# Kernel optimization log

Measured on AMD Instinct MI355X. Metric: run time of the kernel, lower is better.

Reference implementation:

```python
import jax, jax.numpy as jnp
import numpy as np

CIN, COUT, R, N, B = 4, 4, 4, 4096, 32

def setup_inputs() -> dict:
    key = jax.random.key(0)
    k1, k2, k3 = jax.random.split(key, 3)
    x = jax.random.normal(k1, (CIN, B, N), dtype=jnp.float32)
    # torch.nn.init.normal(std=0.01)
    G = 0.01 * jax.random.normal(k2, (CIN, COUT, R, N), dtype=jnp.float32)
    H = 0.01 * jax.random.normal(k3, (CIN, COUT, R, N), dtype=jnp.float32)
    return {"x": x, "G": G, "H": H}

def reference(x, G, H):
    """LDR layer, displacement='toep_corner' (cycle=True).

    For each channel pair (i,j):
        M_ij = sum_s C_1(G[i,j,s]) @ C_{-1}(H[i,j,s])^T
    where C_f(v) is the f-circulant matrix with first column v
    (= Krylov matrix of the f-unit-circulant shift Z_f with vector v).
    out[j] = sum_i M_ij @ x[i]^T  (batched over batch dim).

    Identities used (F = DFT):
      C_1(u) y      = ifft(fft(u) * fft(y))
      C_1(u)^T y    = fft(fft(u) * ifft(y))
      C_f(v)        = D^{-1} C_1(D v) D,  D = diag(zeta^k), zeta = f^{1/n}
      => C_{-1}(h)^T y = D * fft(fft(D*h) * ifft(conj(D)*y)), D_k = exp(i*pi*k/n)
    All channel pairs and ranks are batched in a single FFT call (no Python
    loops over channels, unlike the original double loop).
    """
    cin, b, n = x.shape
    k = jnp.arange(n)
    D = jnp.exp(1j * jnp.pi * k / n).astype(jnp.complex64)   # zeta^k for f=-1
    Dinv = jnp.conj(D)

    # --- step 1: t[i,j,s,b,:] = C_{-1}(H[i,j,s])^T x[i,b,:]  -> (cin,cout,r,b,n)
    Hf = jnp.fft.fft(D * H.astype(jnp.complex64), axis=-1)           # (cin,cout,r,n)
    Xf = jnp.fft.ifft(Dinv * x.astype(jnp.complex64), axis=-1)       # (cin,b,n)
    t = D * jnp.fft.fft(Hf[:, :, :, None, :] * Xf[:, None, None, :, :], axis=-1)

    # --- step 2: out[j,b,:] = Re ifft( sum_{i,s} fft(G[i,j,s]) * fft(t[i,j,s,b]) )
    Gf = jnp.fft.fft(G, axis=-1).astype(jnp.complex64)               # (cin,cout,r,n)
    Tf = jnp.fft.fft(t, axis=-1)                                     # (cin,cout,r,b,n)
    Yf = jnp.einsum('ijsn,ijsbn->jbn', Gf, Tf)                       # (cout,b,n)
    return jnp.real(jnp.fft.ifft(Yf, axis=-1)).astype(x.dtype)
```

## Files before the change

### kernel.cpp

```cpp
#include <hip/hip_runtime.h>
#include <hip/hip_fp16.h>
#include <math.h>


#define NFFT  4096
#define NT    256
#define CIN   4
#define COUT  4
#define RANK  4
#define BATCH 32
#define PI_F  3.14159265358979323846f

constexpr float CP16[16] = {
    1.0000000000000000f,  0.9807852804032304f,  0.9238795325112867f,  0.8314696123025452f,
    0.7071067811865476f,  0.5555702330196022f,  0.3826834323650898f,  0.1950903220161282f,
    0.0000000000000000f, -0.1950903220161282f, -0.3826834323650898f, -0.5555702330196022f,
   -0.7071067811865476f, -0.8314696123025452f, -0.9238795325112867f, -0.9807852804032304f };
constexpr float SP16[16] = {
    0.0000000000000000f,  0.1950903220161282f,  0.3826834323650898f,  0.5555702330196022f,
    0.7071067811865476f,  0.8314696123025452f,  0.9238795325112867f,  0.9807852804032304f,
    1.0000000000000000f,  0.9807852804032304f,  0.9238795325112867f,  0.8314696123025452f,
    0.7071067811865476f,  0.5555702330196022f,  0.3826834323650898f,  0.1950903220161282f };

__device__ __forceinline__ float2 cmul(float2 a, float2 b) {
    return make_float2(a.x*b.x - a.y*b.y, a.x*b.y + a.y*b.x);
}
__device__ __forceinline__ float2 cadd(float2 a, float2 b){ return make_float2(a.x+b.x, a.y+b.y); }
__device__ __forceinline__ float2 csub(float2 a, float2 b){ return make_float2(a.x-b.x, a.y-b.y); }

__device__ __forceinline__ int SW(int e){ return e ^ ((e >> 4) & 15); }

template<int SIGN>
__device__ __forceinline__ void dft16(float2 v[16]) {
    const float sgn = (float)SIGN;
    const float C8 = 0.923879532511287f, S8 = 0.382683432365090f, H2 = 0.707106781186548f;
    const float2 w1 = make_float2( C8,  sgn*S8);
    const float2 w2 = make_float2( H2,  sgn*H2);
    const float2 w3 = make_float2( S8,  sgn*C8);
    const float2 w4 = make_float2(0.f,  sgn);
    const float2 w6 = make_float2(-H2,  sgn*H2);
    const float2 w9 = make_float2(-C8, -sgn*S8);
    float2 t[16];
    #pragma unroll
    for (int p = 0; p < 4; ++p) {
        float2 a0 = v[p], a1 = v[p+4], a2 = v[p+8], a3 = v[p+12];
        float2 b0 = cadd(a0,a2), b1 = csub(a0,a2), b2 = cadd(a1,a3), b3 = csub(a1,a3);
        float2 ib3 = make_float2(-sgn*b3.y, sgn*b3.x);
        float2 X0 = cadd(b0,b2), X2c = csub(b0,b2);
        float2 X1 = cadd(b1,ib3), X3 = csub(b1,ib3);
        if (p == 1) { X1 = cmul(X1,w1); X2c = cmul(X2c,w2); X3 = cmul(X3,w3); }
        else if (p == 2) { X1 = cmul(X1,w2); X2c = cmul(X2c,w4); X3 = cmul(X3,w6); }
        else if (p == 3) { X1 = cmul(X1,w3); X2c = cmul(X2c,w6); X3 = cmul(X3,w9); }
        t[4*p+0]=X0; t[4*p+1]=X1; t[4*p+2]=X2c; t[4*p+3]=X3;
    }
    #pragma unroll
    for (int q = 0; q < 4; ++q) {
        float2 a0 = t[q], a1 = t[q+4], a2 = t[q+8], a3 = t[q+12];
        float2 b0 = cadd(a0,a2), b1 = csub(a0,a2), b2 = cadd(a1,a3), b3 = csub(a1,a3);
        float2 ib3 = make_float2(-sgn*b3.y, sgn*b3.x);
        v[q+0]  = cadd(b0,b2);
        v[q+8]  = csub(b0,b2);
        v[q+4]  = cadd(b1,ib3);
        v[q+12] = csub(b1,ib3);
    }
}

__device__ __forceinline__ void twiddle16(float2 v[16], float ang) {
    float sn, cs; __sincosf(ang, &sn, &cs);
    float2 w  = make_float2(cs, sn);
    float2 w2 = cmul(w, w);
    float2 to = w;
    float2 te = w2;
    v[1] = cmul(v[1], to);
    v[2] = cmul(v[2], te);
    #pragma unroll
    for (int k = 3; k < 16; k += 2) {
        to = cmul(to, w2); v[k] = cmul(v[k], to);
        if (k + 1 < 16) { te = cmul(te, w2); v[k+1] = cmul(v[k+1], te); }
    }
}

__device__ __forceinline__ void twiddle16_pair(float2 v0[16], float2 v1[16], float ang) {
    float sn, cs; __sincosf(ang, &sn, &cs);
    float2 w  = make_float2(cs, sn);
    float2 w2 = cmul(w, w);
    float2 to = w;
    float2 te = w2;
    v0[1] = cmul(v0[1], to); v1[1] = cmul(v1[1], to);
    v0[2] = cmul(v0[2], te); v1[2] = cmul(v1[2], te);
    #pragma unroll
    for (int k = 3; k < 16; k += 2) {
        to = cmul(to, w2); v0[k] = cmul(v0[k], to); v1[k] = cmul(v1[k], to);
        if (k + 1 < 16) { te = cmul(te, w2); v0[k+1] = cmul(v0[k+1], te); v1[k+1] = cmul(v1[k+1], te); }
    }
}

template<int SIGN>
__device__ void fft4096_r16(float2 v[16], float2* lds, int tid) {
    dft16<SIGN>(v);
    twiddle16(v, (float)SIGN * 2.0f * PI_F * (float)tid / 4096.0f);
    #pragma unroll
    for (int k = 0; k < 16; ++k) lds[SW(16*tid + k)] = v[k];
    __syncthreads();
    #pragma unroll
    for (int r = 0; r < 16; ++r) v[r] = lds[SW(tid + 256*r)];
    dft16<SIGN>(v);
    twiddle16(v, (float)SIGN * 2.0f * PI_F * (float)(tid >> 4) / 256.0f);
    __syncthreads();
    {
        const int q = tid & 15, p = tid >> 4;
        #pragma unroll
        for (int k = 0; k < 16; ++k) lds[SW(q + 256*p + 16*k)] = v[k];
    }
    __syncthreads();
    #pragma unroll
    for (int r = 0; r < 16; ++r) v[r] = lds[SW(tid + 256*r)];
    dft16<SIGN>(v);
    __syncthreads();
}

template<int SIGN>
__device__ void fft4096_pair(float2 v0[16], float2 v1[16],
                             float2* lds0, float2* lds1, int tid) {
    dft16<SIGN>(v0);
    dft16<SIGN>(v1);
    twiddle16_pair(v0, v1, (float)SIGN * 2.0f * PI_F * (float)tid / 4096.0f);
    #pragma unroll
    for (int k = 0; k < 16; ++k) {
        const int a = SW(16*tid + k);
        lds0[a] = v0[k]; lds1[a] = v1[k];
    }
    __syncthreads();
    #pragma unroll
    for (int r = 0; r < 16; ++r) {
        const int a = SW(tid + 256*r);
        v0[r] = lds0[a]; v1[r] = lds1[a];
    }
    dft16<SIGN>(v0);
    dft16<SIGN>(v1);
    twiddle16_pair(v0, v1, (float)SIGN * 2.0f * PI_F * (float)(tid >> 4) / 256.0f);
    __syncthreads();
    {
        const int q = tid & 15, p = tid >> 4;
        #pragma unroll
        for (int k = 0; k < 16; ++k) {
            const int a = SW(q + 256*p + 16*k);
            lds0[a] = v0[k]; lds1[a] = v1[k];
        }
    }
    __syncthreads();
    #pragma unroll
    for (int r = 0; r < 16; ++r) {
        const int a = SW(tid + 256*r);
        v0[r] = lds0[a]; v1[r] = lds1[a];
    }
    dft16<SIGN>(v0);
    dft16<SIGN>(v1);
    __syncthreads();
}

__global__ __launch_bounds__(NT, 2) void ldr_pre_k(
    const float* __restrict__ x, const float* __restrict__ G, const float* __restrict__ H,
    float2* __restrict__ Hc, float2* __restrict__ Gf, float2* __restrict__ Xf)
{
    __shared__ float2 lds[NFFT];
    const int tid = threadIdx.x;
    const int bid = blockIdx.x;
    float2 v[16];
    if (bid < 32) {
        const float* h0 = H + (size_t)(2*bid)     * NFFT;
        const float* h1 = H + (size_t)(2*bid + 1) * NFFT;
        float sn, cs; __sincosf(PI_F * (float)tid / (float)NFFT, &sn, &cs);
        const float2 dt = make_float2(cs, sn);
        #pragma unroll
        for (int k = 0; k < 16; ++k) {
            const int e = tid + 256*k;
            const float2 d = cmul(dt, make_float2(CP16[k], SP16[k]));
            v[k] = cmul(d, make_float2(h0[e], h1[e]));
        }
        fft4096_r16<-1>(v, lds, tid);
        float2* o = Hc + (size_t)bid * NFFT;
        #pragma unroll
        for (int k = 0; k < 16; ++k) o[tid + 256*k] = v[k];
    } else if (bid < 96) {
        const int row = bid - 32;
        const float* g = G + (size_t)row * NFFT;
        #pragma unroll
        for (int k = 0; k < 16; ++k) v[k] = make_float2(g[tid + 256*k], 0.0f);
        fft4096_r16<-1>(v, lds, tid);
        float2* o = Gf + (size_t)row * NFFT;
        #pragma unroll
        for (int k = 0; k < 16; ++k) o[tid + 256*k] = v[k];
    } else {
        const int row = bid - 96;
        const float* xp = x + (size_t)row * NFFT;
        float sn, cs; __sincosf(PI_F * (float)tid / (float)NFFT, &sn, &cs);
        const float2 dt = make_float2(cs, -sn);
        #pragma unroll
        for (int k = 0; k < 16; ++k) {
            const int e = tid + 256*k;
            const float2 d = cmul(dt, make_float2(CP16[k], -SP16[k]));
            float xv = xp[e];
            v[k] = make_float2(d.x*xv, d.y*xv);
        }
        fft4096_r16<1>(v, lds, tid);
        const float invn = 1.0f / (float)NFFT;
        float2* o = Xf + (size_t)row * NFFT;
        #pragma unroll
        for (int k = 0; k < 16; ++k) o[tid + 256*k] = make_float2(v[k].x*invn, v[k].y*invn);
    }
}

__global__ __launch_bounds__(NT, 2) void ldr_mid_k(
    const float2* __restrict__ Hc, const float2* __restrict__ Xf,
    const float2* __restrict__ Gf, __half2* __restrict__ Ph)
{
    __shared__ float2 lds0[NFFT];
    __shared__ float2 lds1[NFFT];
    const int tid = threadIdx.x;
    const int bid = blockIdx.x;
    const int bp  = bid & 15;
    const int ip  = bid >> 4;
    const int pr  = ip & 1;
    const int ij  = ip >> 1;
    const int i   = ij >> 2;
    const int j   = ij & 3;
    const int r0  = ij*RANK + 2*pr;
    const int b0  = 2*bp;
    const float2* hc = Hc + (size_t)ip * NFFT;
    const float2* x0 = Xf + (size_t)(i*BATCH + b0) * NFFT;
    const float2* x1 = x0 + NFFT;
    const float2* g0 = Gf + (size_t)r0 * NFFT;
    const float2* g1 = g0 + NFFT;
    const int u = i*2 + pr;

    float2 v0[16], v1[16];
    #pragma unroll
    for (int k = 0; k < 16; ++k) {
        const int e = tid + 256*k;
        const float2 h = hc[e];
        v0[k] = cmul(h, x0[e]);
        v1[k] = cmul(h, x1[e]);
    }
    fft4096_pair<-1>(v0, v1, lds0, lds1, tid);
    {
        float sn, cs; __sincosf(PI_F * (float)tid / (float)NFFT, &sn, &cs);
        const float2 dt = make_float2(cs, sn);
        #pragma unroll
        for (int k = 0; k < 16; ++k) {
            const float2 d = cmul(dt, make_float2(CP16[k], SP16[k]));
            v0[k] = cmul(v0[k], d);
            v1[k] = cmul(v1[k], d);
        }
    }
    fft4096_pair<-1>(v0, v1, lds0, lds1, tid);

    #pragma unroll
    for (int k = 8; k < 16; ++k) {
        const int a = SW(tid + 256*k);
        lds0[a] = v0[k]; lds1[a] = v1[k];
    }
    __syncthreads();

    __half2* prow0 = Ph + (size_t)((u*COUT + j)*BATCH + b0) * (NFFT/2);
    __half2* prow1 = prow0 + (NFFT/2);
    #pragma unroll
    for (int k = 0; k < 8; ++k) {
        const int e = tid + 256*k;
        const float2 g0e = g0[e], g1e = g1[e];
        const int am = SW(4096 - e);
        {
            const float2 Zk = v0[k];
            const float2 Zm = (e == 0) ? Zk : lds0[am];
            const float2 V1 = make_float2(0.5f*(Zk.x + Zm.x), 0.5f*(Zk.y - Zm.y));
            const float2 V2 = make_float2(0.5f*(Zk.y + Zm.y), 0.5f*(Zm.x - Zk.x));
            float2 Y = cadd(cmul(g0e, V1), cmul(g1e, V2));
            if (k == 0 && tid == 0) {
                const float2 Zn = v0[8];
                const float Ynyq = g0[2048].x * Zn.x + g1[2048].x * Zn.y;
                Y = make_float2(Y.x, Ynyq);
            }
            prow0[e] = __floats2half2_rn(Y.x, Y.y);
        }
        {
            const float2 Zk = v1[k];
            const float2 Zm = (e == 0) ? Zk : lds1[am];
            const float2 V1 = make_float2(0.5f*(Zk.x + Zm.x), 0.5f*(Zk.y - Zm.y));
            const float2 V2 = make_float2(0.5f*(Zk.y + Zm.y), 0.5f*(Zm.x - Zk.x));
            float2 Y = cadd(cmul(g0e, V1), cmul(g1e, V2));
            if (k == 0 && tid == 0) {
                const float2 Zn = v1[8];
                const float Ynyq = g0[2048].x * Zn.x + g1[2048].x * Zn.y;
                Y = make_float2(Y.x, Ynyq);
            }
            prow1[e] = __floats2half2_rn(Y.x, Y.y);
        }
    }
}

__global__ __launch_bounds__(NT, 2) void ldr_fin_k(
    const __half2* __restrict__ Ph, float* __restrict__ out)
{
    __shared__ float2 lds[NFFT];
    __shared__ float2 sh[NFFT/2];
    const int tid = threadIdx.x;
    const int bid = blockIdx.x;
    const int b = bid & (BATCH - 1);
    const int j = bid >> 5;

    float2 a[8];
    #pragma unroll
    for (int k = 0; k < 8; ++k) a[k] = make_float2(0.f, 0.f);
    #pragma unroll
    for (int u = 0; u < 8; ++u) {
        const int4* row4 = (const int4*)(Ph + (size_t)((u*COUT + j)*BATCH + b) * (NFFT/2));
        #pragma unroll
        for (int c = 0; c < 2; ++c) {
            const int4 w = row4[tid + 256*c];
            const int ww[4] = { w.x, w.y, w.z, w.w };
            #pragma unroll
            for (int r = 0; r < 4; ++r) {
                __half2 h = *(const __half2*)&ww[r];
                float2 f = __half22float2(h);
                a[c*4+r] = cadd(a[c*4+r], f);
            }
        }
    }
    float4* sh4 = (float4*)sh;
    #pragma unroll
    for (int c = 0; c < 2; ++c) {
        sh4[2*(tid + 256*c) + 0] = make_float4(a[c*4+0].x, a[c*4+0].y, a[c*4+1].x, a[c*4+1].y);
        sh4[2*(tid + 256*c) + 1] = make_float4(a[c*4+2].x, a[c*4+2].y, a[c*4+3].x, a[c*4+3].y);
    }
    __syncthreads();

    const float dc  = sh[0].x;
    const float nyq = sh[0].y;
    float2 v[16];
    #pragma unroll
    for (int k = 0; k < 8; ++k) v[k] = sh[tid + 256*k];
    if (tid == 0) v[0] = make_float2(dc, 0.0f);
    #pragma unroll
    for (int k = 8; k < 16; ++k) {
        const int m = 4096 - (tid + 256*k);
        if (m == 2048) {
            v[k] = make_float2(nyq, 0.0f);
        } else {
            float2 c = sh[m];
            v[k] = make_float2(c.x, -c.y);
        }
    }
    fft4096_r16<1>(v, lds, tid);
    const float invn = 1.0f / (float)NFFT;
    float* orow = out + (size_t)bid * NFFT;
    #pragma unroll
    for (int k = 0; k < 16; ++k) orow[tid + 256*k] = v[k].x * invn;
}

extern "C" void kernel_launch(void* const* d_in, const int* in_sizes, int n_in,
                              void* d_out, int out_size, void* d_ws, size_t ws_size,
                              hipStream_t stream) {
    const float* x = (const float*)d_in[0];
    const float* G = (const float*)d_in[1];
    const float* H = (const float*)d_in[2];
    float* out = (float*)d_out;

    float2*  Hc = (float2*)d_ws;
    float2*  Gf = Hc + (size_t)32 * NFFT;
    float2*  Xf = Gf + (size_t)64 * NFFT;
    __half2* Ph = (__half2*)(Xf + (size_t)128 * NFFT);

    ldr_pre_k<<<224, NT, 0, stream>>>(x, G, H, Hc, Gf, Xf);
    ldr_mid_k<<<512, NT, 0, stream>>>(Hc, Xf, Gf, Ph);
    ldr_fin_k<<<COUT * BATCH, NT, 0, stream>>>(Ph, out);
}
```

Measured before the change: 93.86 us.

## Switch mid kernel to 512-thread radix-8 paired FFT

Rewrites the middle kernel's two paired 4096-point FFTs from a radix-16, 256-thread, 3-pass scheme to a radix-8, 512-thread, 4-pass scheme. Each thread now holds 8 elements per signal instead of 16, which cuts register pressure and doubles threads per block to raise occupancy and latency hiding. The cost is an extra LDS exchange pass and barrier per FFT, plus reworked indexing for the load, twiddle and real-split epilogue.

```diff
diff --git a/kernel.cpp b/kernel.cpp
--- a/kernel.cpp
+++ b/kernel.cpp
@@ -5,6 +5,7 @@
 
 #define NFFT  4096
 #define NT    256
+#define NTM   512
 #define CIN   4
 #define COUT  4
 #define RANK  4
@@ -21,6 +22,12 @@
     0.7071067811865476f,  0.8314696123025452f,  0.9238795325112867f,  0.9807852804032304f,
     1.0000000000000000f,  0.9807852804032304f,  0.9238795325112867f,  0.8314696123025452f,
     0.7071067811865476f,  0.5555702330196022f,  0.3826834323650898f,  0.1950903220161282f };
+constexpr float CP8[8] = {
+    1.0000000000000000f,  0.9238795325112867f,  0.7071067811865476f,  0.3826834323650898f,
+    0.0000000000000000f, -0.3826834323650898f, -0.7071067811865476f, -0.9238795325112867f };
+constexpr float SP8[8] = {
+    0.0000000000000000f,  0.3826834323650898f,  0.7071067811865476f,  0.9238795325112867f,
+    1.0000000000000000f,  0.9238795325112867f,  0.7071067811865476f,  0.3826834323650898f };
 
 __device__ __forceinline__ float2 cmul(float2 a, float2 b) {
     return make_float2(a.x*b.x - a.y*b.y, a.x*b.y + a.y*b.x);
@@ -80,7 +87,54 @@
     }
 }
 
-__device__ __forceinline__ void twiddle16_pair(float2 v0[16], float2 v1[16], float ang) {
+template<int SIGN>
+__device__ void fft4096_r16(float2 v[16], float2* lds, int tid) {
+    dft16<SIGN>(v);
+    twiddle16(v, (float)SIGN * 2.0f * PI_F * (float)tid / 4096.0f);
+    #pragma unroll
+    for (int k = 0; k < 16; ++k) lds[SW(16*tid + k)] = v[k];
+    __syncthreads();
+    #pragma unroll
+    for (int r = 0; r < 16; ++r) v[r] = lds[SW(tid + 256*r)];
+    dft16<SIGN>(v);
+    twiddle16(v, (float)SIGN * 2.0f * PI_F * (float)(tid >> 4) / 256.0f);
+    __syncthreads();
+    {
+        const int q = tid & 15, p = tid >> 4;
+        #pragma unroll
+        for (int k = 0; k < 16; ++k) lds[SW(q + 256*p + 16*k)] = v[k];
+    }
+    __syncthreads();
+    #pragma unroll
+    for (int r = 0; r < 16; ++r) v[r] = lds[SW(tid + 256*r)];
+    dft16<SIGN>(v);
+    __syncthreads();
+}
+
+template<int SIGN>
+__device__ __forceinline__ void dft8(float2 v[8]) {
+    const float sgn = (float)SIGN;
+    const float H2 = 0.707106781186548f;
+    float2 a0 = v[0], a1 = v[2], a2 = v[4], a3 = v[6];
+    float2 b0 = cadd(a0,a2), b1 = csub(a0,a2), b2 = cadd(a1,a3), b3 = csub(a1,a3);
+    float2 ib3 = make_float2(-sgn*b3.y, sgn*b3.x);
+    float2 E0 = cadd(b0,b2), E2 = csub(b0,b2), E1 = cadd(b1,ib3), E3 = csub(b1,ib3);
+    a0 = v[1]; a1 = v[3]; a2 = v[5]; a3 = v[7];
+    b0 = cadd(a0,a2); b1 = csub(a0,a2); b2 = cadd(a1,a3); b3 = csub(a1,a3);
+    ib3 = make_float2(-sgn*b3.y, sgn*b3.x);
+    float2 O0 = cadd(b0,b2), O2 = csub(b0,b2), O1 = cadd(b1,ib3), O3 = csub(b1,ib3);
+    const float2 w1 = make_float2( H2,  sgn*H2);
+    const float2 w3 = make_float2(-H2,  sgn*H2);
+    O1 = cmul(O1, w1);
+    O2 = make_float2(-sgn*O2.y, sgn*O2.x);
+    O3 = cmul(O3, w3);
+    v[0] = cadd(E0,O0); v[4] = csub(E0,O0);
+    v[1] = cadd(E1,O1); v[5] = csub(E1,O1);
+    v[2] = cadd(E2,O2); v[6] = csub(E2,O2);
+    v[3] = cadd(E3,O3); v[7] = csub(E3,O3);
+}
+
+__device__ __forceinline__ void twiddle8_pair(float2 v0[8], float2 v1[8], float ang) {
     float sn, cs; __sincosf(ang, &sn, &cs);
     float2 w  = make_float2(cs, sn);
     float2 w2 = cmul(w, w);
@@ -88,74 +142,64 @@
     float2 te = w2;
     v0[1] = cmul(v0[1], to); v1[1] = cmul(v1[1], to);
     v0[2] = cmul(v0[2], te); v1[2] = cmul(v1[2], te);
-    #pragma unroll
-    for (int k = 3; k < 16; k += 2) {
-        to = cmul(to, w2); v0[k] = cmul(v0[k], to); v1[k] = cmul(v1[k], to);
-        if (k + 1 < 16) { te = cmul(te, w2); v0[k+1] = cmul(v0[k+1], te); v1[k+1] = cmul(v1[k+1], te); }
-    }
+    to = cmul(to, w2); v0[3] = cmul(v0[3], to); v1[3] = cmul(v1[3], to);
+    te = cmul(te, w2); v0[4] = cmul(v0[4], te); v1[4] = cmul(v1[4], te);
+    to = cmul(to, w2); v0[5] = cmul(v0[5], to); v1[5] = cmul(v1[5], to);
+    te = cmul(te, w2); v0[6] = cmul(v0[6], te); v1[6] = cmul(v1[6], te);
+    to = cmul(to, w2); v0[7] = cmul(v0[7], to); v1[7] = cmul(v1[7], to);
 }
 
 template<int SIGN>
-__device__ void fft4096_r16(float2 v[16], float2* lds, int tid) {
-    dft16<SIGN>(v);
-    twiddle16(v, (float)SIGN * 2.0f * PI_F * (float)tid / 4096.0f);
-    #pragma unroll
-    for (int k = 0; k < 16; ++k) lds[SW(16*tid + k)] = v[k];
-    __syncthreads();
-    #pragma unroll
-    for (int r = 0; r < 16; ++r) v[r] = lds[SW(tid + 256*r)];
-    dft16<SIGN>(v);
-    twiddle16(v, (float)SIGN * 2.0f * PI_F * (float)(tid >> 4) / 256.0f);
+__device__ void fft4096_r8_pair(float2 v0[8], float2 v1[8],
+                                float2* lds0, float2* lds1, int tid) {
+    dft8<SIGN>(v0); dft8<SIGN>(v1);
+    twiddle8_pair(v0, v1, (float)SIGN * 2.0f * PI_F * (float)tid / 4096.0f);
+    #pragma unroll
+    for (int k = 0; k < 8; ++k) {
+        const int a = SW(8*tid + k);
+        lds0[a] = v0[k]; lds1[a] = v1[k];
+    }
+    __syncthreads();
+    #pragma unroll
+    for (int r = 0; r < 8; ++r) {
+        const int a = SW(tid + 512*r);
+        v0[r] = lds0[a]; v1[r] = lds1[a];
+    }
+    dft8<SIGN>(v0); dft8<SIGN>(v1);
+    twiddle8_pair(v0, v1, (float)SIGN * 2.0f * PI_F * (float)(tid >> 3) / 512.0f);
     __syncthreads();
     {
-        const int q = tid & 15, p = tid >> 4;
-        #pragma unroll
-        for (int k = 0; k < 16; ++k) lds[SW(q + 256*p + 16*k)] = v[k];
-    }
-    __syncthreads();
-    #pragma unroll
-    for (int r = 0; r < 16; ++r) v[r] = lds[SW(tid + 256*r)];
-    dft16<SIGN>(v);
-    __syncthreads();
-}
-
-template<int SIGN>
-__device__ void fft4096_pair(float2 v0[16], float2 v1[16],
-                             float2* lds0, float2* lds1, int tid) {
-    dft16<SIGN>(v0);
-    dft16<SIGN>(v1);
-    twiddle16_pair(v0, v1, (float)SIGN * 2.0f * PI_F * (float)tid / 4096.0f);
-    #pragma unroll
-    for (int k = 0; k < 16; ++k) {
-        const int a = SW(16*tid + k);
-        lds0[a] = v0[k]; lds1[a] = v1[k];
-    }
-    __syncthreads();
-    #pragma unroll
-    for (int r = 0; r < 16; ++r) {
-        const int a = SW(tid + 256*r);
+        const int base = (tid & 7) + 64*(tid >> 3);
+        #pragma unroll
+        for (int k = 0; k < 8; ++k) {
+            const int a = SW(base + 8*k);
+            lds0[a] = v0[k]; lds1[a] = v1[k];
+        }
+    }
+    __syncthreads();
+    #pragma unroll
+    for (int r = 0; r < 8; ++r) {
+        const int a = SW(tid + 512*r);
         v0[r] = lds0[a]; v1[r] = lds1[a];
     }
-    dft16<SIGN>(v0);
-    dft16<SIGN>(v1);
-    twiddle16_pair(v0, v1, (float)SIGN * 2.0f * PI_F * (float)(tid >> 4) / 256.0f);
+    dft8<SIGN>(v0); dft8<SIGN>(v1);
+    twiddle8_pair(v0, v1, (float)SIGN * 2.0f * PI_F * (float)(tid >> 6) / 64.0f);
     __syncthreads();
     {
-        const int q = tid & 15, p = tid >> 4;
-        #pragma unroll
-        for (int k = 0; k < 16; ++k) {
-            const int a = SW(q + 256*p + 16*k);
+        const int base = (tid & 63) + 512*(tid >> 6);
+        #pragma unroll
+        for (int k = 0; k < 8; ++k) {
+            const int a = SW(base + 64*k);
             lds0[a] = v0[k]; lds1[a] = v1[k];
         }
     }
     __syncthreads();
     #pragma unroll
-    for (int r = 0; r < 16; ++r) {
-        const int a = SW(tid + 256*r);
+    for (int r = 0; r < 8; ++r) {
+        const int a = SW(tid + 512*r);
         v0[r] = lds0[a]; v1[r] = lds1[a];
     }
-    dft16<SIGN>(v0);
-    dft16<SIGN>(v1);
+    dft8<SIGN>(v0); dft8<SIGN>(v1);
     __syncthreads();
 }
 
@@ -211,7 +255,7 @@
     }
 }
 
-__global__ __launch_bounds__(NT, 2) void ldr_mid_k(
+__global__ __launch_bounds__(NTM, 2) void ldr_mid_k(
     const float2* __restrict__ Hc, const float2* __restrict__ Xf,
     const float2* __restrict__ Gf, __half2* __restrict__ Ph)
 {
@@ -234,30 +278,30 @@
     const float2* g1 = g0 + NFFT;
     const int u = i*2 + pr;
 
-    float2 v0[16], v1[16];
-    #pragma unroll
-    for (int k = 0; k < 16; ++k) {
-        const int e = tid + 256*k;
+    float2 v0[8], v1[8];
+    #pragma unroll
+    for (int k = 0; k < 8; ++k) {
+        const int e = tid + NTM*k;
         const float2 h = hc[e];
         v0[k] = cmul(h, x0[e]);
         v1[k] = cmul(h, x1[e]);
     }
-    fft4096_pair<-1>(v0, v1, lds0, lds1, tid);
+    fft4096_r8_pair<-1>(v0, v1, lds0, lds1, tid);
     {
         float sn, cs; __sincosf(PI_F * (float)tid / (float)NFFT, &sn, &cs);
         const float2 dt = make_float2(cs, sn);
         #pragma unroll
-        for (int k = 0; k < 16; ++k) {
-            const float2 d = cmul(dt, make_float2(CP16[k], SP16[k]));
+        for (int k = 0; k < 8; ++k) {
+            const float2 d = cmul(dt, make_float2(CP8[k], SP8[k]));
             v0[k] = cmul(v0[k], d);
             v1[k] = cmul(v1[k], d);
         }
     }
-    fft4096_pair<-1>(v0, v1, lds0, lds1, tid);
-
-    #pragma unroll
-    for (int k = 8; k < 16; ++k) {
-        const int a = SW(tid + 256*k);
+    fft4096_r8_pair<-1>(v0, v1, lds0, lds1, tid);
+
+    #pragma unroll
+    for (int k = 4; k < 8; ++k) {
+        const int a = SW(tid + NTM*k);
         lds0[a] = v0[k]; lds1[a] = v1[k];
     }
     __syncthreads();
@@ -265,18 +309,19 @@
     __half2* prow0 = Ph + (size_t)((u*COUT + j)*BATCH + b0) * (NFFT/2);
     __half2* prow1 = prow0 + (NFFT/2);
     #pragma unroll
-    for (int k = 0; k < 8; ++k) {
-        const int e = tid + 256*k;
+    for (int k = 0; k < 4; ++k) {
+        const int e = tid + NTM*k;
         const float2 g0e = g0[e], g1e = g1[e];
-        const int am = SW(4096 - e);
         {
             const float2 Zk = v0[k];
-            const float2 Zm = (e == 0) ? Zk : lds0[am];
+            float2 Zm;
+            if (e == 0) Zm = Zk;
+            else        Zm = lds0[SW(4096 - e)];
             const float2 V1 = make_float2(0.5f*(Zk.x + Zm.x), 0.5f*(Zk.y - Zm.y));
             const float2 V2 = make_float2(0.5f*(Zk.y + Zm.y), 0.5f*(Zm.x - Zk.x));
             float2 Y = cadd(cmul(g0e, V1), cmul(g1e, V2));
             if (k == 0 && tid == 0) {
-                const float2 Zn = v0[8];
+                const float2 Zn = v0[4];
                 const float Ynyq = g0[2048].x * Zn.x + g1[2048].x * Zn.y;
                 Y = make_float2(Y.x, Ynyq);
             }
@@ -284,12 +329,14 @@
         }
         {
             const float2 Zk = v1[k];
-            const float2 Zm = (e == 0) ? Zk : lds1[am];
+            float2 Zm;
+            if (e == 0) Zm = Zk;
+            else        Zm = lds1[SW(4096 - e)];
             const float2 V1 = make_float2(0.5f*(Zk.x + Zm.x), 0.5f*(Zk.y - Zm.y));
             const float2 V2 = make_float2(0.5f*(Zk.y + Zm.y), 0.5f*(Zm.x - Zk.x));
             float2 Y = cadd(cmul(g0e, V1), cmul(g1e, V2));
             if (k == 0 && tid == 0) {
-                const float2 Zn = v1[8];
+                const float2 Zn = v1[4];
                 const float Ynyq = g0[2048].x * Zn.x + g1[2048].x * Zn.y;
                 Y = make_float2(Y.x, Ynyq);
             }
@@ -371,6 +418,6 @@
     __half2* Ph = (__half2*)(Xf + (size_t)128 * NFFT);
 
     ldr_pre_k<<<224, NT, 0, stream>>>(x, G, H, Hc, Gf, Xf);
-    ldr_mid_k<<<512, NT, 0, stream>>>(Hc, Xf, Gf, Ph);
+    ldr_mid_k<<<512, NTM, 0, stream>>>(Hc, Xf, Gf, Ph);
     ldr_fin_k<<<COUT * BATCH, NT, 0, stream>>>(Ph, out);
 }
```

Measured after the change: 94.07 us. Within noise of the previous version (+0.2%).
